# Performance work log

Hardware: AMD Instinct MI355X
Metric: run time of the kernel (lower is better)

Reference implementation:

```python
import jax, jax.numpy as jnp
import numpy as np

D_MODEL = 1024
N_HEADS = 16
POINT_DIM = 4
PLUCKER_DIM = 6
PAIRS4 = [(0, 1), (0, 2), (0, 3), (1, 2), (1, 3), (2, 3)]
_J6 = jnp.array([[0, 0, 0, 0, 0, 1], [0, 0, 0, 0, -1, 0], [0, 0, 0, 1, 0, 0],
                 [0, 0, 1, 0, 0, 0], [0, -1, 0, 0, 0, 0], [1, 0, 0, 0, 0, 0]], dtype=jnp.float32)


def exterior(p1, p2):
    # p1, p2: [..., point_dim] -> normalized Plucker coords [..., 6]
    L = jnp.stack([p1[..., i] * p2[..., j] - p1[..., j] * p2[..., i] for i, j in PAIRS4], axis=-1)
    n = jnp.linalg.norm(L, axis=-1, keepdims=True)
    return L / jnp.maximum(n, 1e-12)


def setup_inputs() -> dict:
    key = jax.random.key(0)
    ks = jax.random.split(key, 16)
    B, T, D, H, pd = 2, 1024, D_MODEL, N_HEADS, POINT_DIM
    s = 0.02
    return {
        "x": jax.random.normal(ks[0], (B, T, D), dtype=jnp.float32),
        "qkv_w": jax.random.normal(ks[1], (D, 3 * D), dtype=jnp.float32) * s,
        "qkv_b": jnp.zeros((3 * D,), dtype=jnp.float32),
        "w1_write_w": jax.random.normal(ks[2], (2 * D, pd * H), dtype=jnp.float32) * s,
        "w2_write_w": jax.random.normal(ks[3], (D, pd * H), dtype=jnp.float32) * s,
        "w1_read_w": jax.random.normal(ks[4], (D, pd * H), dtype=jnp.float32) * s,
        "w2_read_w": jax.random.normal(ks[5], (D, pd * H), dtype=jnp.float32) * s,
        "mem_value_w": jax.random.normal(ks[6], (D, D), dtype=jnp.float32) * s,
        "mem_value_b": jnp.zeros((D,), dtype=jnp.float32),
        "mem_gate_w": jax.random.normal(ks[7], (D, H), dtype=jnp.float32) * s,
        "mem_gate_b": jnp.zeros((H,), dtype=jnp.float32),
        "mem_scale": jnp.full((H,), 0.1, dtype=jnp.float32),
        "out_w": jax.random.normal(ks[8], (D, D), dtype=jnp.float32) * s,
        "out_b": jnp.zeros((D,), dtype=jnp.float32),
        "decay_logits": jnp.full((H,), 4.6, dtype=jnp.float32),
        "J": _J6,
    }


def reference(x, qkv_w, qkv_b, w1_write_w, w2_write_w, w1_read_w, w2_read_w,
              mem_value_w, mem_value_b, mem_gate_w, mem_gate_b, mem_scale,
              out_w, out_b, decay_logits, J):
    B, T, D = x.shape
    H = N_HEADS
    dh = D // H
    pd = POINT_DIM
    scale = dh ** (-0.5)

    # ---- standard causal attention ----
    qkv = (x @ qkv_w + qkv_b).reshape(B, T, 3, H, dh)
    q = jnp.transpose(qkv[:, :, 0], (0, 2, 1, 3))  # [B,H,T,dh]
    k = jnp.transpose(qkv[:, :, 1], (0, 2, 1, 3))
    v = jnp.transpose(qkv[:, :, 2], (0, 2, 1, 3))
    scores = jnp.einsum('bhtd,bhsd->bhts', q, k) * scale
    causal_mask = jnp.triu(jnp.ones((T, T), dtype=bool), k=1)
    scores = jnp.where(causal_mask, -jnp.inf, scores)
    attn = jax.nn.softmax(scores, axis=-1)
    seq_out = jnp.einsum('bhts,bhsd->bthd', attn, v).reshape(B, T, D)

    # ---- trigram write lines ----
    z = jnp.zeros((B, 1, D), dtype=x.dtype)
    x_prev1 = jnp.concatenate([z, x[:, :-1]], axis=1)
    x_prev2 = jnp.concatenate([z, z, x[:, :-2]], axis=1)
    trigram_ctx = jnp.concatenate([x_prev2, x_prev1], axis=-1)  # [B,T,2D]
    w1 = (trigram_ctx @ w1_write_w).reshape(B, T, H, pd)
    w2 = (x @ w2_write_w).reshape(B, T, H, pd)
    write_lines = exterior(w1, w2)  # [B,T,H,6]
    r1 = (x @ w1_read_w).reshape(B, T, H, pd)
    r2 = (x @ w2_read_w).reshape(B, T, H, pd)
    read_lines = exterior(r1, r2)  # [B,T,H,6]

    # ---- Plucker incidence + decay weighting ----
    J_write = jnp.einsum('bshi,ij->bshj', write_lines, J)
    incidence = jnp.einsum('bthi,bshi->bhts', read_lines, J_write)  # [B,H,T,T]
    incidence_sq = incidence ** 2
    positions = jnp.arange(T, dtype=x.dtype)
    diffs = positions[:, None] - positions[None, :]  # [T,T]
    decays = jax.nn.sigmoid(decay_logits)  # [H]
    # strictly-causal (diffs>0) decay weights; masked_fill(triu diag=0, 0) == (diffs>0)
    weights = jnp.where(diffs[None] > 0, decays[:, None, None] ** jnp.maximum(diffs, 0.0)[None], 0.0)
    mem_score = jnp.sum(incidence_sq * weights[None], axis=-1)  # [B,H,T]

    # ---- gated memory value ----
    mem_val = x @ mem_value_w + mem_value_b  # [B,T,D]
    gate = jax.nn.sigmoid(x @ mem_gate_w + mem_gate_b)  # [B,T,H]
    mem_score_t = jnp.transpose(mem_score, (0, 2, 1))  # [B,T,H]
    gated = jax.nn.sigmoid(mem_score_t * mem_scale[None, None, :]) * gate
    gated = jnp.mean(gated, axis=-1, keepdims=True)  # [B,T,1]

    return (seq_out + gated * mem_val) @ out_w + out_b
```

## Files before the change

### kernel.cpp

```cpp
#include <hip/hip_runtime.h>
#include <hip/hip_bf16.h>
#include <stdint.h>


typedef __attribute__((ext_vector_type(8))) __bf16 bf16v8;
typedef __attribute__((ext_vector_type(8))) short  s16x8;
typedef __attribute__((ext_vector_type(4))) float  f32x4;

#define LOG2E 1.4426950408889634f

__device__ __forceinline__ float bf2f(short s) {
  union { uint32_t u; float f; } cv; cv.u = ((uint32_t)(uint16_t)s) << 16; return cv.f;
}
__device__ __forceinline__ short f2bf(float f) {
  union { float f; uint32_t u; } cv; cv.f = f;
  uint32_t r = cv.u + 0x7fffu + ((cv.u >> 16) & 1u);
  return (short)(r >> 16);
}

__device__ __forceinline__ f32x4 mfma_bf16(s16x8 a, s16x8 b, f32x4 c) {
  return __builtin_amdgcn_mfma_f32_16x16x32_bf16(
      __builtin_bit_cast(bf16v8, a), __builtin_bit_cast(bf16v8, b), c, 0, 0, 0);
}

__device__ __forceinline__ void gload_lds16(const void* g, void* l) {
  __builtin_amdgcn_global_load_lds(
      (const __attribute__((address_space(1))) uint32_t*)g,
      (__attribute__((address_space(3))) uint32_t*)l, 16, 0, 0);
}


__global__ void k_cvt(const float* __restrict__ in, short* __restrict__ out, int n) {
  int i = (blockIdx.x * 256 + threadIdx.x) * 4;
  if (i < n) {
    float4 v = *(const float4*)&in[i];
    short4 o;
    o.x = f2bf(v.x); o.y = f2bf(v.y); o.z = f2bf(v.z); o.w = f2bf(v.w);
    *(short4*)&out[i] = o;
  }
}

__global__ void k_tconv(const float* __restrict__ W, short* __restrict__ Wt, int K, int N) {
  __shared__ float tile[32][33];
  const int n0 = blockIdx.x * 32, k0 = blockIdx.y * 32;
  const int tx = threadIdx.x, ty = threadIdx.y;
#pragma unroll
  for (int i = 0; i < 4; i++)
    tile[ty + i * 8][tx] = W[(size_t)(k0 + ty + i * 8) * N + n0 + tx];
  __syncthreads();
#pragma unroll
  for (int i = 0; i < 4; i++)
    Wt[(size_t)(n0 + ty + i * 8) * K + k0 + tx] = f2bf(tile[tx][ty + i * 8]);
}

__global__ void k_smallw(const float* __restrict__ w1w, const float* __restrict__ w2w,
                         const float* __restrict__ r1w, const float* __restrict__ r2w,
                         const float* __restrict__ gw, const float* __restrict__ qkvb,
                         const float* __restrict__ mvb, short* __restrict__ out,
                         float* __restrict__ biasAll) {
  if (blockIdx.x >= 1536) {
    const int i = (blockIdx.x - 1536) * 256 + threadIdx.x;
    if (i < 4480) {
      float v = 0.f;
      if (i < 3072) v = qkvb[i];
      else if (i < 4096) v = mvb[i - 3072];
      biasAll[i] = v;
    }
    return;
  }
  const int idx = blockIdx.x * 256 + threadIdx.x;
  const int r = idx >> 10, k = idx & 1023;
  float v = 0.f;
  if (r < 64)       v = w1w[(size_t)k * 64 + r];
  else if (r < 128) v = w1w[(size_t)(1024 + k) * 64 + (r - 64)];
  else if (r < 192) v = w2w[(size_t)k * 64 + (r - 128)];
  else if (r < 256) v = r1w[(size_t)k * 64 + (r - 192)];
  else if (r < 320) v = r2w[(size_t)k * 64 + (r - 256)];
  else if (r < 336) v = gw[(size_t)k * 16 + (r - 320)];
  out[idx] = f2bf(v);
}


__global__ __launch_bounds__(256) void k_gemmF(const short* __restrict__ A,
                                               const short* __restrict__ Bt,
                                               short* __restrict__ C,
                                               const float* __restrict__ bias,
                                               float* __restrict__ projf) {
  const int N = 4480, K = 1024;
  __shared__ short As[128 * 32];
  __shared__ short Bs[128 * 32];
  const int m0 = blockIdx.x * 128, n0 = blockIdx.y * 128;
  const int tid = threadIdx.x;
  const int lane = tid & 63, w = tid >> 6;
  const int wr = (w >> 1) * 64, wc = (w & 1) * 64;
  const int l15 = lane & 15, lg = lane >> 4;
  f32x4 acc[4][4] = {};
  for (int k0 = 0; k0 < K; k0 += 32) {
#pragma unroll
    for (int p = 0; p < 2; p++) {
      const int e = p * 256 + tid;
      const int r = e >> 2, c8 = (e & 3) << 3;
      gload_lds16(A + (size_t)(m0 + r) * K + k0 + c8, As + e * 8);
      gload_lds16(Bt + (size_t)(n0 + r) * K + k0 + c8, Bs + e * 8);
    }
    __syncthreads();
    s16x8 af[4], bfv[4];
#pragma unroll
    for (int i = 0; i < 4; i++) {
      af[i]  = *(const s16x8*)&As[(wr + i * 16 + l15) * 32 + lg * 8];
      bfv[i] = *(const s16x8*)&Bs[(wc + i * 16 + l15) * 32 + lg * 8];
    }
#pragma unroll
    for (int mi = 0; mi < 4; mi++)
#pragma unroll
      for (int ni = 0; ni < 4; ni++)
        acc[mi][ni] = mfma_bf16(af[mi], bfv[ni], acc[mi][ni]);
    __syncthreads();
  }
  const bool isproj = (n0 >= 4096);
#pragma unroll
  for (int mi = 0; mi < 4; mi++)
#pragma unroll
    for (int ni = 0; ni < 4; ni++) {
      const int col = n0 + wc + ni * 16 + l15;
      const float bv = bias[col];
#pragma unroll
      for (int r = 0; r < 4; r++) {
        const int row = m0 + wr + mi * 16 + lg * 4 + r;
        const float v = acc[mi][ni][r] + bv;
        if (isproj) projf[(size_t)row * 384 + (col - 4096)] = v;
        else        C[(size_t)row * 4480 + col] = f2bf(v);
      }
    }
}


__global__ __launch_bounds__(256) void k_gemm(const short* __restrict__ A,
                                              const short* __restrict__ Bt,
                                              float* __restrict__ C,
                                              const float* __restrict__ bias,
                                              int N, int K) {
  __shared__ short As[128 * 32];
  __shared__ short Bs[128 * 32];
  const int m0 = blockIdx.x * 128, n0 = blockIdx.y * 128;
  const int tid = threadIdx.x;
  const int lane = tid & 63, w = tid >> 6;
  const int wr = (w >> 1) * 64, wc = (w & 1) * 64;
  const int l15 = lane & 15, lg = lane >> 4;
  f32x4 acc[4][4] = {};
  for (int k0 = 0; k0 < K; k0 += 32) {
#pragma unroll
    for (int p = 0; p < 2; p++) {
      const int e = p * 256 + tid;
      const int r = e >> 2, c8 = (e & 3) << 3;
      gload_lds16(A + (size_t)(m0 + r) * K + k0 + c8, As + e * 8);
      gload_lds16(Bt + (size_t)(n0 + r) * K + k0 + c8, Bs + e * 8);
    }
    __syncthreads();
    s16x8 af[4], bfv[4];
#pragma unroll
    for (int i = 0; i < 4; i++) {
      af[i]  = *(const s16x8*)&As[(wr + i * 16 + l15) * 32 + lg * 8];
      bfv[i] = *(const s16x8*)&Bs[(wc + i * 16 + l15) * 32 + lg * 8];
    }
#pragma unroll
    for (int mi = 0; mi < 4; mi++)
#pragma unroll
      for (int ni = 0; ni < 4; ni++)
        acc[mi][ni] = mfma_bf16(af[mi], bfv[ni], acc[mi][ni]);
    __syncthreads();
  }
#pragma unroll
  for (int mi = 0; mi < 4; mi++)
#pragma unroll
    for (int ni = 0; ni < 4; ni++) {
      const int col = n0 + wc + ni * 16 + l15;
      const float bv = bias ? bias[col] : 0.f;
#pragma unroll
      for (int r = 0; r < 4; r++) {
        const int row = m0 + wr + mi * 16 + lg * 4 + r;
        C[(size_t)row * N + col] = acc[mi][ni][r] + bv;
      }
    }
}


__global__ void k_vtr(const short* __restrict__ fused, short* __restrict__ vtg) {
  __shared__ short tile[32][33];
  const int bh = blockIdx.z;
  const int b = bh >> 4, h = bh & 15;
  const int t0 = blockIdx.x * 32, d0 = blockIdx.y * 32;
  const int tx = threadIdx.x, ty = threadIdx.y;
#pragma unroll
  for (int i = 0; i < 4; i++)
    tile[ty + i * 8][tx] =
        fused[(size_t)(b * 1024 + t0 + ty + i * 8) * 4480 + 2048 + h * 64 + d0 + tx];
  __syncthreads();
#pragma unroll
  for (int i = 0; i < 4; i++)
    vtg[(size_t)(bh * 64 + d0 + ty + i * 8) * 1024 + t0 + tx] = tile[tx][ty + i * 8];
}


__global__ __launch_bounds__(256) void k_attn(const short* __restrict__ fused,
                                              const short* __restrict__ vtg,
                                              short* __restrict__ outp) {
  const int id = blockIdx.x;
  const int phase = id >> 8;
  const int v = id & 255;
  const int bh = (v & 7) + 8 * ((v >> 3) & 3);
  const int jx = v >> 5;
  const int j = phase ? jx : (15 - jx);
  const int b = bh >> 4, h = bh & 15;
  const int tid = threadIdx.x, lane = tid & 63, w = tid >> 6;
  const int l15 = lane & 15, lg = lane >> 4;
  const int q0 = j * 64;
  const int nkv = j + 1;

  __shared__ short Kl[2][64 * 72];
  __shared__ short Vt[2][64 * 72];
  __shared__ short Pl[4][16 * 72];
  const short* base = fused + (size_t)b * 1024 * 4480;
  const short* vbase = vtg + (size_t)bh * 64 * 1024;
  short* op = outp + (size_t)b * 1024 * 1024;

  const int e0 = tid, e1 = tid + 256;
  const int r0e = e0 >> 3, c0e = (e0 & 7) << 3;
  const int r1e = e1 >> 3, c1e = (e1 & 7) << 3;

  s16x8 qf[2];
#pragma unroll
  for (int ks = 0; ks < 2; ks++)
    qf[ks] = *(const s16x8*)&base[(size_t)(q0 + w * 16 + l15) * 4480 +
                                  h * 64 + ks * 32 + lg * 8];

  f32x4 O[4] = {};
  float m_run[4], l_run[4];
#pragma unroll
  for (int r = 0; r < 4; r++) { m_run[r] = -1e30f; l_run[r] = 0.f; }

  {
    s16x8 ka = *(const s16x8*)&base[(size_t)r0e * 4480 + 1024 + h * 64 + c0e];
    s16x8 kb = *(const s16x8*)&base[(size_t)r1e * 4480 + 1024 + h * 64 + c1e];
    s16x8 va = *(const s16x8*)&vbase[(size_t)r0e * 1024 + c0e];
    s16x8 vb = *(const s16x8*)&vbase[(size_t)r1e * 1024 + c1e];
    *(s16x8*)&Kl[0][r0e * 72 + c0e] = ka;
    *(s16x8*)&Kl[0][r1e * 72 + c1e] = kb;
    *(s16x8*)&Vt[0][r0e * 72 + c0e] = va;
    *(s16x8*)&Vt[0][r1e * 72 + c1e] = vb;
  }
  __syncthreads();

  for (int kt = 0; kt < nkv; kt++) {
    const int cur = kt & 1;
    const int kv0 = kt * 64;
    const bool pf = (kt + 1 < nkv);
    s16x8 kn0, kn1, vn0, vn1;
    if (pf) {
      const int kvn = kv0 + 64;
      kn0 = *(const s16x8*)&base[(size_t)(kvn + r0e) * 4480 + 1024 + h * 64 + c0e];
      kn1 = *(const s16x8*)&base[(size_t)(kvn + r1e) * 4480 + 1024 + h * 64 + c1e];
      vn0 = *(const s16x8*)&vbase[(size_t)r0e * 1024 + kvn + c0e];
      vn1 = *(const s16x8*)&vbase[(size_t)r1e * 1024 + kvn + c1e];
    }

    f32x4 S[4] = {};
    __builtin_amdgcn_s_setprio(1);
#pragma unroll
    for (int sf = 0; sf < 4; sf++) {
      s16x8 kf0 = *(const s16x8*)&Kl[cur][(sf * 16 + l15) * 72 + lg * 8];
      s16x8 kf1 = *(const s16x8*)&Kl[cur][(sf * 16 + l15) * 72 + 32 + lg * 8];
      S[sf] = mfma_bf16(qf[0], kf0, S[sf]);
      S[sf] = mfma_bf16(qf[1], kf1, S[sf]);
    }
    __builtin_amdgcn_s_setprio(0);

    const bool diag = (kt == j);
    float sv[4][4];
#pragma unroll
    for (int sf = 0; sf < 4; sf++)
#pragma unroll
      for (int r = 0; r < 4; r++) {
        float vv = S[sf][r] * 0.125f;
        if (diag) {
          const int sg = kv0 + sf * 16 + l15;
          const int qg = q0 + w * 16 + lg * 4 + r;
          if (sg > qg) vv = -1e30f;
        }
        sv[sf][r] = vv;
      }
#pragma unroll
    for (int r = 0; r < 4; r++) {
      float pm = fmaxf(fmaxf(sv[0][r], sv[1][r]), fmaxf(sv[2][r], sv[3][r]));
      pm = fmaxf(pm, __shfl_xor(pm, 1, 64));
      pm = fmaxf(pm, __shfl_xor(pm, 2, 64));
      pm = fmaxf(pm, __shfl_xor(pm, 4, 64));
      pm = fmaxf(pm, __shfl_xor(pm, 8, 64));
      const float mn = fmaxf(m_run[r], pm);
      const float fac = exp2f((m_run[r] - mn) * LOG2E);
      m_run[r] = mn;
      float rs = 0.f;
#pragma unroll
      for (int sf = 0; sf < 4; sf++) {
        float p = (sv[sf][r] <= -1e29f) ? 0.f : exp2f((sv[sf][r] - mn) * LOG2E);
        rs += p;
        Pl[w][(lg * 4 + r) * 72 + sf * 16 + l15] = f2bf(p);
      }
      rs += __shfl_xor(rs, 1, 64);
      rs += __shfl_xor(rs, 2, 64);
      rs += __shfl_xor(rs, 4, 64);
      rs += __shfl_xor(rs, 8, 64);
      l_run[r] = l_run[r] * fac + rs;
#pragma unroll
      for (int nf = 0; nf < 4; nf++) O[nf][r] *= fac;
    }

    __builtin_amdgcn_s_setprio(1);
#pragma unroll
    for (int ks = 0; ks < 2; ks++) {
      s16x8 pfr = *(const s16x8*)&Pl[w][l15 * 72 + ks * 32 + lg * 8];
#pragma unroll
      for (int nf = 0; nf < 4; nf++) {
        s16x8 vf = *(const s16x8*)&Vt[cur][(nf * 16 + l15) * 72 + ks * 32 + lg * 8];
        O[nf] = mfma_bf16(pfr, vf, O[nf]);
      }
    }
    __builtin_amdgcn_s_setprio(0);

    __syncthreads();
    if (pf) {
      const int nxt = cur ^ 1;
      *(s16x8*)&Kl[nxt][r0e * 72 + c0e] = kn0;
      *(s16x8*)&Kl[nxt][r1e * 72 + c1e] = kn1;
      *(s16x8*)&Vt[nxt][r0e * 72 + c0e] = vn0;
      *(s16x8*)&Vt[nxt][r1e * 72 + c1e] = vn1;
      __syncthreads();
    }
  }

#pragma unroll
  for (int nf = 0; nf < 4; nf++)
#pragma unroll
    for (int r = 0; r < 4; r++) {
      const int row = q0 + w * 16 + lg * 4 + r;
      op[(size_t)row * 1024 + h * 64 + nf * 16 + l15] = f2bf(O[nf][r] / l_run[r]);
    }
}


__device__ __forceinline__ void exterior6(const float p1[4], const float p2[4], float L[6]) {
  L[0] = p1[0] * p2[1] - p1[1] * p2[0];
  L[1] = p1[0] * p2[2] - p1[2] * p2[0];
  L[2] = p1[0] * p2[3] - p1[3] * p2[0];
  L[3] = p1[1] * p2[2] - p1[2] * p2[1];
  L[4] = p1[1] * p2[3] - p1[3] * p2[1];
  L[5] = p1[2] * p2[3] - p1[3] * p2[2];
  float n = sqrtf(L[0] * L[0] + L[1] * L[1] + L[2] * L[2] +
                  L[3] * L[3] + L[4] * L[4] + L[5] * L[5]);
  float inv = 1.f / fmaxf(n, 1e-12f);
#pragma unroll
  for (int j = 0; j < 6; j++) L[j] *= inv;
}

__global__ void k_lines(const float* __restrict__ proj, const float* __restrict__ Jm,
                        float* __restrict__ jw, float* __restrict__ rl) {
  const int idx = blockIdx.x * 256 + threadIdx.x;
  const int t = idx & 1023, h = (idx >> 10) & 15, b = idx >> 14;
  const int n = b * 1024 + t;
  const int bh = b * 16 + h;
  float p1[4], p2[4], L[6];
#pragma unroll
  for (int p = 0; p < 4; p++) {
    float a  = (t >= 2) ? proj[(size_t)(n - 2) * 384 + h * 4 + p] : 0.f;
    float bb = (t >= 1) ? proj[(size_t)(n - 1) * 384 + 64 + h * 4 + p] : 0.f;
    p1[p] = a + bb;
    p2[p] = proj[(size_t)n * 384 + 128 + h * 4 + p];
  }
  exterior6(p1, p2, L);
  const size_t jo = (size_t)bh * 6144 + t;
#pragma unroll
  for (int j = 0; j < 6; j++) {
    float s = 0.f;
#pragma unroll
    for (int i = 0; i < 6; i++) s += L[i] * Jm[i * 6 + j];
    jw[jo + (size_t)j * 1024] = s;
  }
#pragma unroll
  for (int p = 0; p < 4; p++) {
    p1[p] = proj[(size_t)n * 384 + 192 + h * 4 + p];
    p2[p] = proj[(size_t)n * 384 + 256 + h * 4 + p];
  }
  exterior6(p1, p2, L);
  const size_t ro = ((size_t)bh * 1024 + t) * 6;
#pragma unroll
  for (int j = 0; j < 6; j++) rl[ro + j] = L[j];
}


__global__ __launch_bounds__(256) void k_mscore(const float* __restrict__ jw,
                                                const float* __restrict__ rl,
                                                const float* __restrict__ dlog,
                                                float* __restrict__ ms) {
  const int gtid = blockIdx.x * 256 + threadIdx.x;
  const int wid = gtid >> 6, lane = gtid & 63;
  const int bh = wid >> 10, t = wid & 1023;
  const int h = bh & 15, b = bh >> 4;
  const float d = 1.f / (1.f + expf(-dlog[h]));
  const float l2d = log2f(d);
  const float* jwp = jw + (size_t)bh * 6144;
  const float* rp = rl + ((size_t)bh * 1024 + t) * 6;
  const float r0 = rp[0], r1 = rp[1], r2 = rp[2], r3 = rp[3], r4 = rp[4], r5 = rp[5];
  float wgt = exp2f((float)(t - lane) * l2d);
  const float gw = exp2f(-64.f * l2d);
  float acc = 0.f;
  for (int s = lane; s < t; s += 64) {
    const float dot = r0 * jwp[s] + r1 * jwp[1024 + s] + r2 * jwp[2048 + s] +
                      r3 * jwp[3072 + s] + r4 * jwp[4096 + s] + r5 * jwp[5120 + s];
    acc += wgt * dot * dot;
    wgt *= gw;
  }
  acc += __shfl_xor(acc, 1, 64);
  acc += __shfl_xor(acc, 2, 64);
  acc += __shfl_xor(acc, 4, 64);
  acc += __shfl_xor(acc, 8, 64);
  acc += __shfl_xor(acc, 16, 64);
  acc += __shfl_xor(acc, 32, 64);
  if (lane == 0) ms[((size_t)(b * 1024 + t)) * 16 + h] = acc;
}


__global__ __launch_bounds__(256) void k_combine(const short* __restrict__ attn,
                                                 const short* __restrict__ fused,
                                                 const float* __restrict__ proj,
                                                 const float* __restrict__ ms,
                                                 const float* __restrict__ mem_scale,
                                                 const float* __restrict__ gate_b,
                                                 short* __restrict__ comb) {
  const int n = blockIdx.x;
  const int tid = threadIdx.x;
  __shared__ float gsh;
  if (tid < 16) {
    const float gp = proj[(size_t)n * 384 + 320 + tid] + gate_b[tid];
    const float g = 1.f / (1.f + expf(-gp));
    const float sc = ms[(size_t)n * 16 + tid] * mem_scale[tid];
    const float sg = 1.f / (1.f + expf(-sc));
    float v = sg * g;
    v += __shfl_xor(v, 1, 64);
    v += __shfl_xor(v, 2, 64);
    v += __shfl_xor(v, 4, 64);
    v += __shfl_xor(v, 8, 64);
    if (tid == 0) gsh = v * (1.f / 16.f);
  }
  __syncthreads();
  const float g = gsh;
  const int c0 = tid * 4;
  short4 av = *(const short4*)&attn[(size_t)n * 1024 + c0];
  short4 mvv = *(const short4*)&fused[(size_t)n * 4480 + 3072 + c0];
  short4 ov;
  ov.x = f2bf(bf2f(av.x) + g * bf2f(mvv.x));
  ov.y = f2bf(bf2f(av.y) + g * bf2f(mvv.y));
  ov.z = f2bf(bf2f(av.z) + g * bf2f(mvv.z));
  ov.w = f2bf(bf2f(av.w) + g * bf2f(mvv.w));
  *(short4*)&comb[(size_t)n * 1024 + c0] = ov;
}


extern "C" void kernel_launch(void* const* d_in, const int* in_sizes, int n_in,
                              void* d_out, int out_size, void* d_ws, size_t ws_size,
                              hipStream_t stream) {
  const float* x    = (const float*)d_in[0];
  const float* qkvw = (const float*)d_in[1];
  const float* qkvb = (const float*)d_in[2];
  const float* w1w  = (const float*)d_in[3];
  const float* w2w  = (const float*)d_in[4];
  const float* r1w  = (const float*)d_in[5];
  const float* r2w  = (const float*)d_in[6];
  const float* mvw  = (const float*)d_in[7];
  const float* mvb  = (const float*)d_in[8];
  const float* gw   = (const float*)d_in[9];
  const float* gb   = (const float*)d_in[10];
  const float* msc  = (const float*)d_in[11];
  const float* ow   = (const float*)d_in[12];
  const float* ob   = (const float*)d_in[13];
  const float* dlog = (const float*)d_in[14];
  const float* Jm   = (const float*)d_in[15];
  float* out = (float*)d_out;

  char* wsp = (char*)d_ws;
  auto alloc = [&](size_t bytes) {
    char* p = wsp;
    wsp += (bytes + 255) & ~(size_t)255;
    return p;
  };
  short* xb     = (short*)alloc((size_t)2048 * 1024 * 2);
  short* btall  = (short*)alloc((size_t)4480 * 1024 * 2);
  short* owT    = (short*)alloc((size_t)1024 * 1024 * 2);
  short* fusedC = (short*)alloc((size_t)2048 * 4480 * 2);
  float* projf  = (float*)alloc((size_t)2048 * 384 * 4);
  float* biasA  = (float*)alloc((size_t)4480 * 4);
  short* vtg    = (short*)alloc((size_t)32 * 64 * 1024 * 2);
  short* attnO  = (short*)alloc((size_t)2048 * 1024 * 2);
  short* comb   = (short*)alloc((size_t)2048 * 1024 * 2);
  float* jwb    = (float*)alloc((size_t)32 * 6144 * 4);
  float* rlb    = (float*)alloc((size_t)32768 * 6 * 4);
  float* msb    = (float*)alloc((size_t)2048 * 16 * 4);

  k_cvt<<<2048, 256, 0, stream>>>(x, xb, 2048 * 1024);
  dim3 tb(32, 8);
  k_tconv<<<dim3(96, 32), tb, 0, stream>>>(qkvw, btall, 1024, 3072);
  k_tconv<<<dim3(32, 32), tb, 0, stream>>>(mvw, btall + (size_t)3072 * 1024, 1024, 1024);
  k_tconv<<<dim3(32, 32), tb, 0, stream>>>(ow, owT, 1024, 1024);
  k_smallw<<<1554, 256, 0, stream>>>(w1w, w2w, r1w, r2w, gw, qkvb, mvb,
                                     btall + (size_t)4096 * 1024, biasA);

  k_gemmF<<<dim3(16, 35), 256, 0, stream>>>(xb, btall, fusedC, biasA, projf);

  k_vtr<<<dim3(32, 2, 32), tb, 0, stream>>>(fusedC, vtg);
  k_attn<<<512, 256, 0, stream>>>(fusedC, vtg, attnO);

  k_lines<<<128, 256, 0, stream>>>(projf, Jm, jwb, rlb);
  k_mscore<<<8192, 256, 0, stream>>>(jwb, rlb, dlog, msb);
  k_combine<<<2048, 256, 0, stream>>>(attnO, fusedC, projf, msb, msc, gb, comb);

  k_gemm<<<dim3(16, 8), 256, 0, stream>>>(comb, owT, out, ob, 1024, 1024);
}
```

Before: 143.7 us.

## Split attention KV range across two blocks, merge partials, fuse prep kernels

Attention now runs as 1024 blocks, each handling half of a query tile's causal KV range. A new merge kernel combines the two float partial outputs using their saved max and sum statistics, which shortens the longest blocks and raises parallelism. The online softmax now rescales only when the running max grows by more than a threshold, and the LDS K/V tiles are single-buffered. The five weight and input conversion launches are folded into one prep kernel to cut launch overhead, at the cost of extra float partial traffic and a further launch for the merge.

```diff
diff --git a/kernel.cpp b/kernel.cpp
--- a/kernel.cpp
+++ b/kernel.cpp
@@ -30,54 +30,65 @@
 }
 
 
-__global__ void k_cvt(const float* __restrict__ in, short* __restrict__ out, int n) {
-  int i = (blockIdx.x * 256 + threadIdx.x) * 4;
-  if (i < n) {
-    float4 v = *(const float4*)&in[i];
+__global__ __launch_bounds__(256) void k_prep(
+    const float* __restrict__ x, const float* __restrict__ qkvw,
+    const float* __restrict__ mvw, const float* __restrict__ ow,
+    const float* __restrict__ w1w, const float* __restrict__ w2w,
+    const float* __restrict__ r1w, const float* __restrict__ r2w,
+    const float* __restrict__ gw, const float* __restrict__ qkvb,
+    const float* __restrict__ mvb,
+    short* __restrict__ xb, short* __restrict__ btall, short* __restrict__ owT,
+    float* __restrict__ biasAll) {
+  __shared__ float tile[32][33];
+  const int bid = blockIdx.x;
+  const int tid = threadIdx.x;
+  if (bid < 2048) {
+    const int i = (bid * 256 + tid) * 4;
+    float4 v = *(const float4*)&x[i];
     short4 o;
     o.x = f2bf(v.x); o.y = f2bf(v.y); o.z = f2bf(v.z); o.w = f2bf(v.w);
-    *(short4*)&out[i] = o;
-  }
-}
-
-__global__ void k_tconv(const float* __restrict__ W, short* __restrict__ Wt, int K, int N) {
-  __shared__ float tile[32][33];
-  const int n0 = blockIdx.x * 32, k0 = blockIdx.y * 32;
-  const int tx = threadIdx.x, ty = threadIdx.y;
-#pragma unroll
-  for (int i = 0; i < 4; i++)
-    tile[ty + i * 8][tx] = W[(size_t)(k0 + ty + i * 8) * N + n0 + tx];
-  __syncthreads();
-#pragma unroll
-  for (int i = 0; i < 4; i++)
-    Wt[(size_t)(n0 + ty + i * 8) * K + k0 + tx] = f2bf(tile[tx][ty + i * 8]);
-}
-
-__global__ void k_smallw(const float* __restrict__ w1w, const float* __restrict__ w2w,
-                         const float* __restrict__ r1w, const float* __restrict__ r2w,
-                         const float* __restrict__ gw, const float* __restrict__ qkvb,
-                         const float* __restrict__ mvb, short* __restrict__ out,
-                         float* __restrict__ biasAll) {
-  if (blockIdx.x >= 1536) {
-    const int i = (blockIdx.x - 1536) * 256 + threadIdx.x;
+    *(short4*)&xb[i] = o;
+    return;
+  }
+  if (bid < 7168) {
+    const float* W; short* Wt; int N, u;
+    if (bid < 5120)      { W = qkvw; Wt = btall;                       N = 3072; u = bid - 2048; }
+    else if (bid < 6144) { W = mvw;  Wt = btall + (size_t)3072 * 1024; N = 1024; u = bid - 5120; }
+    else                 { W = ow;   Wt = owT;                         N = 1024; u = bid - 6144; }
+    const int ntiles = N >> 5;
+    const int n0 = (u % ntiles) * 32, k0 = (u / ntiles) * 32;
+    const int tx = tid & 31, ty = tid >> 5;
+#pragma unroll
+    for (int i = 0; i < 4; i++)
+      tile[ty + i * 8][tx] = W[(size_t)(k0 + ty + i * 8) * N + n0 + tx];
+    __syncthreads();
+#pragma unroll
+    for (int i = 0; i < 4; i++)
+      Wt[(size_t)(n0 + ty + i * 8) * 1024 + k0 + tx] = f2bf(tile[tx][ty + i * 8]);
+    return;
+  }
+  if (bid < 8704) {
+    const int idx = (bid - 7168) * 256 + tid;
+    const int r = idx >> 10, k = idx & 1023;
+    float v = 0.f;
+    if (r < 64)       v = w1w[(size_t)k * 64 + r];
+    else if (r < 128) v = w1w[(size_t)(1024 + k) * 64 + (r - 64)];
+    else if (r < 192) v = w2w[(size_t)k * 64 + (r - 128)];
+    else if (r < 256) v = r1w[(size_t)k * 64 + (r - 192)];
+    else if (r < 320) v = r2w[(size_t)k * 64 + (r - 256)];
+    else if (r < 336) v = gw[(size_t)k * 16 + (r - 320)];
+    btall[(size_t)4096 * 1024 + idx] = f2bf(v);
+    return;
+  }
+  {
+    const int i = (bid - 8704) * 256 + tid;
     if (i < 4480) {
       float v = 0.f;
       if (i < 3072) v = qkvb[i];
       else if (i < 4096) v = mvb[i - 3072];
       biasAll[i] = v;
     }
-    return;
-  }
-  const int idx = blockIdx.x * 256 + threadIdx.x;
-  const int r = idx >> 10, k = idx & 1023;
-  float v = 0.f;
-  if (r < 64)       v = w1w[(size_t)k * 64 + r];
-  else if (r < 128) v = w1w[(size_t)(1024 + k) * 64 + (r - 64)];
-  else if (r < 192) v = w2w[(size_t)k * 64 + (r - 128)];
-  else if (r < 256) v = r1w[(size_t)k * 64 + (r - 192)];
-  else if (r < 320) v = r2w[(size_t)k * 64 + (r - 256)];
-  else if (r < 336) v = gw[(size_t)k * 16 + (r - 320)];
-  out[idx] = f2bf(v);
+  }
 }
 
 
@@ -204,25 +215,27 @@
 
 __global__ __launch_bounds__(256) void k_attn(const short* __restrict__ fused,
                                               const short* __restrict__ vtg,
-                                              short* __restrict__ outp) {
+                                              float* __restrict__ Of,
+                                              float* __restrict__ Ml) {
   const int id = blockIdx.x;
-  const int phase = id >> 8;
-  const int v = id & 255;
-  const int bh = (v & 7) + 8 * ((v >> 3) & 3);
-  const int jx = v >> 5;
-  const int j = phase ? jx : (15 - jx);
+  const int j = 15 - (id >> 6);
+  const int rem = id & 63;
+  const int sid = rem >> 5, bh = rem & 31;
   const int b = bh >> 4, h = bh & 15;
   const int tid = threadIdx.x, lane = tid & 63, w = tid >> 6;
   const int l15 = lane & 15, lg = lane >> 4;
   const int q0 = j * 64;
   const int nkv = j + 1;
-
-  __shared__ short Kl[2][64 * 72];
-  __shared__ short Vt[2][64 * 72];
+  const int half = (nkv + 1) >> 1;
+  const int lo = sid ? half : 0;
+  const int hi = sid ? nkv : half;
+  const int pidx = ((j * 32 + bh) << 1) | sid;
+
+  __shared__ short Kl[64 * 72];
+  __shared__ short Vt[64 * 72];
   __shared__ short Pl[4][16 * 72];
   const short* base = fused + (size_t)b * 1024 * 4480;
   const short* vbase = vtg + (size_t)bh * 64 * 1024;
-  short* op = outp + (size_t)b * 1024 * 1024;
 
   const int e0 = tid, e1 = tid + 256;
   const int r0e = e0 >> 3, c0e = (e0 & 7) << 3;
@@ -239,22 +252,22 @@
 #pragma unroll
   for (int r = 0; r < 4; r++) { m_run[r] = -1e30f; l_run[r] = 0.f; }
 
-  {
-    s16x8 ka = *(const s16x8*)&base[(size_t)r0e * 4480 + 1024 + h * 64 + c0e];
-    s16x8 kb = *(const s16x8*)&base[(size_t)r1e * 4480 + 1024 + h * 64 + c1e];
-    s16x8 va = *(const s16x8*)&vbase[(size_t)r0e * 1024 + c0e];
-    s16x8 vb = *(const s16x8*)&vbase[(size_t)r1e * 1024 + c1e];
-    *(s16x8*)&Kl[0][r0e * 72 + c0e] = ka;
-    *(s16x8*)&Kl[0][r1e * 72 + c1e] = kb;
-    *(s16x8*)&Vt[0][r0e * 72 + c0e] = va;
-    *(s16x8*)&Vt[0][r1e * 72 + c1e] = vb;
+  if (lo < hi) {
+    const int kv0 = lo * 64;
+    s16x8 ka = *(const s16x8*)&base[(size_t)(kv0 + r0e) * 4480 + 1024 + h * 64 + c0e];
+    s16x8 kb = *(const s16x8*)&base[(size_t)(kv0 + r1e) * 4480 + 1024 + h * 64 + c1e];
+    s16x8 va = *(const s16x8*)&vbase[(size_t)r0e * 1024 + kv0 + c0e];
+    s16x8 vb = *(const s16x8*)&vbase[(size_t)r1e * 1024 + kv0 + c1e];
+    *(s16x8*)&Kl[r0e * 72 + c0e] = ka;
+    *(s16x8*)&Kl[r1e * 72 + c1e] = kb;
+    *(s16x8*)&Vt[r0e * 72 + c0e] = va;
+    *(s16x8*)&Vt[r1e * 72 + c1e] = vb;
   }
   __syncthreads();
 
-  for (int kt = 0; kt < nkv; kt++) {
-    const int cur = kt & 1;
+  for (int kt = lo; kt < hi; kt++) {
     const int kv0 = kt * 64;
-    const bool pf = (kt + 1 < nkv);
+    const bool pf = (kt + 1 < hi);
     s16x8 kn0, kn1, vn0, vn1;
     if (pf) {
       const int kvn = kv0 + 64;
@@ -268,8 +281,8 @@
     __builtin_amdgcn_s_setprio(1);
 #pragma unroll
     for (int sf = 0; sf < 4; sf++) {
-      s16x8 kf0 = *(const s16x8*)&Kl[cur][(sf * 16 + l15) * 72 + lg * 8];
-      s16x8 kf1 = *(const s16x8*)&Kl[cur][(sf * 16 + l15) * 72 + 32 + lg * 8];
+      s16x8 kf0 = *(const s16x8*)&Kl[(sf * 16 + l15) * 72 + lg * 8];
+      s16x8 kf1 = *(const s16x8*)&Kl[(sf * 16 + l15) * 72 + 32 + lg * 8];
       S[sf] = mfma_bf16(qf[0], kf0, S[sf]);
       S[sf] = mfma_bf16(qf[1], kf1, S[sf]);
     }
@@ -296,13 +309,17 @@
       pm = fmaxf(pm, __shfl_xor(pm, 2, 64));
       pm = fmaxf(pm, __shfl_xor(pm, 4, 64));
       pm = fmaxf(pm, __shfl_xor(pm, 8, 64));
-      const float mn = fmaxf(m_run[r], pm);
-      const float fac = exp2f((m_run[r] - mn) * LOG2E);
-      m_run[r] = mn;
+      if (pm > m_run[r] + 8.f) {
+        const float fac = exp2f((m_run[r] - pm) * LOG2E);
+        m_run[r] = pm;
+        l_run[r] *= fac;
+#pragma unroll
+        for (int nf = 0; nf < 4; nf++) O[nf][r] *= fac;
+      }
       float rs = 0.f;
 #pragma unroll
       for (int sf = 0; sf < 4; sf++) {
-        float p = (sv[sf][r] <= -1e29f) ? 0.f : exp2f((sv[sf][r] - mn) * LOG2E);
+        float p = (sv[sf][r] <= -1e29f) ? 0.f : exp2f((sv[sf][r] - m_run[r]) * LOG2E);
         rs += p;
         Pl[w][(lg * 4 + r) * 72 + sf * 16 + l15] = f2bf(p);
       }
@@ -310,9 +327,7 @@
       rs += __shfl_xor(rs, 2, 64);
       rs += __shfl_xor(rs, 4, 64);
       rs += __shfl_xor(rs, 8, 64);
-      l_run[r] = l_run[r] * fac + rs;
-#pragma unroll
-      for (int nf = 0; nf < 4; nf++) O[nf][r] *= fac;
+      l_run[r] += rs;
     }
 
     __builtin_amdgcn_s_setprio(1);
@@ -321,7 +336,7 @@
       s16x8 pfr = *(const s16x8*)&Pl[w][l15 * 72 + ks * 32 + lg * 8];
 #pragma unroll
       for (int nf = 0; nf < 4; nf++) {
-        s16x8 vf = *(const s16x8*)&Vt[cur][(nf * 16 + l15) * 72 + ks * 32 + lg * 8];
+        s16x8 vf = *(const s16x8*)&Vt[(nf * 16 + l15) * 72 + ks * 32 + lg * 8];
         O[nf] = mfma_bf16(pfr, vf, O[nf]);
       }
     }
@@ -329,22 +344,55 @@
 
     __syncthreads();
     if (pf) {
-      const int nxt = cur ^ 1;
-      *(s16x8*)&Kl[nxt][r0e * 72 + c0e] = kn0;
-      *(s16x8*)&Kl[nxt][r1e * 72 + c1e] = kn1;
-      *(s16x8*)&Vt[nxt][r0e * 72 + c0e] = vn0;
-      *(s16x8*)&Vt[nxt][r1e * 72 + c1e] = vn1;
+      *(s16x8*)&Kl[r0e * 72 + c0e] = kn0;
+      *(s16x8*)&Kl[r1e * 72 + c1e] = kn1;
+      *(s16x8*)&Vt[r0e * 72 + c0e] = vn0;
+      *(s16x8*)&Vt[r1e * 72 + c1e] = vn1;
       __syncthreads();
     }
   }
 
-#pragma unroll
-  for (int nf = 0; nf < 4; nf++)
-#pragma unroll
-    for (int r = 0; r < 4; r++) {
-      const int row = q0 + w * 16 + lg * 4 + r;
-      op[(size_t)row * 1024 + h * 64 + nf * 16 + l15] = f2bf(O[nf][r] / l_run[r]);
-    }
+  float* ob = Of + (size_t)pidx * 4096;
+  float* mb = Ml + (size_t)pidx * 128;
+#pragma unroll
+  for (int r = 0; r < 4; r++) {
+    const int rloc = w * 16 + lg * 4 + r;
+#pragma unroll
+    for (int nf = 0; nf < 4; nf++)
+      ob[rloc * 64 + nf * 16 + l15] = O[nf][r];
+    if (l15 == 0) {
+      mb[rloc] = m_run[r];
+      mb[64 + rloc] = l_run[r];
+    }
+  }
+}
+
+
+__global__ __launch_bounds__(256) void k_amerge(const float* __restrict__ Of,
+                                                const float* __restrict__ Ml,
+                                                short* __restrict__ outp) {
+  const int g = blockIdx.x * 256 + threadIdx.x;
+  const int rg = g >> 4, c4 = (g & 15) << 2;
+  const int p = rg >> 6, rloc = rg & 63;
+  const int j = p >> 5, bh = p & 31;
+  const int b = bh >> 4, h = bh & 15;
+  const int t = j * 64 + rloc;
+  const float* ml0 = Ml + (size_t)(p * 2 + 0) * 128;
+  const float* ml1 = Ml + (size_t)(p * 2 + 1) * 128;
+  const float m0 = ml0[rloc], l0 = ml0[64 + rloc];
+  const float m1 = ml1[rloc], l1 = ml1[64 + rloc];
+  const float M = fmaxf(m0, m1);
+  const float w0 = exp2f((m0 - M) * LOG2E);
+  const float w1 = exp2f((m1 - M) * LOG2E);
+  const float inv = 1.f / (w0 * l0 + w1 * l1);
+  f32x4 o0 = *(const f32x4*)&Of[(size_t)(p * 2 + 0) * 4096 + rloc * 64 + c4];
+  f32x4 o1 = *(const f32x4*)&Of[(size_t)(p * 2 + 1) * 4096 + rloc * 64 + c4];
+  short4 ov;
+  ov.x = f2bf((w0 * o0[0] + w1 * o1[0]) * inv);
+  ov.y = f2bf((w0 * o0[1] + w1 * o1[1]) * inv);
+  ov.z = f2bf((w0 * o0[2] + w1 * o1[2]) * inv);
+  ov.w = f2bf((w0 * o0[3] + w1 * o1[3]) * inv);
+  *(short4*)&outp[((size_t)(b * 1024 + t)) * 1024 + h * 64 + c4] = ov;
 }
 
 
@@ -504,19 +552,17 @@
   float* jwb    = (float*)alloc((size_t)32 * 6144 * 4);
   float* rlb    = (float*)alloc((size_t)32768 * 6 * 4);
   float* msb    = (float*)alloc((size_t)2048 * 16 * 4);
-
-  k_cvt<<<2048, 256, 0, stream>>>(x, xb, 2048 * 1024);
-  dim3 tb(32, 8);
-  k_tconv<<<dim3(96, 32), tb, 0, stream>>>(qkvw, btall, 1024, 3072);
-  k_tconv<<<dim3(32, 32), tb, 0, stream>>>(mvw, btall + (size_t)3072 * 1024, 1024, 1024);
-  k_tconv<<<dim3(32, 32), tb, 0, stream>>>(ow, owT, 1024, 1024);
-  k_smallw<<<1554, 256, 0, stream>>>(w1w, w2w, r1w, r2w, gw, qkvb, mvb,
-                                     btall + (size_t)4096 * 1024, biasA);
+  float* Of     = (float*)alloc((size_t)1024 * 4096 * 4);
+  float* Mlb    = (float*)alloc((size_t)1024 * 128 * 4);
+
+  k_prep<<<8722, 256, 0, stream>>>(x, qkvw, mvw, ow, w1w, w2w, r1w, r2w, gw,
+                                   qkvb, mvb, xb, btall, owT, biasA);
 
   k_gemmF<<<dim3(16, 35), 256, 0, stream>>>(xb, btall, fusedC, biasA, projf);
 
-  k_vtr<<<dim3(32, 2, 32), tb, 0, stream>>>(fusedC, vtg);
-  k_attn<<<512, 256, 0, stream>>>(fusedC, vtg, attnO);
+  k_vtr<<<dim3(32, 2, 32), dim3(32, 8), 0, stream>>>(fusedC, vtg);
+  k_attn<<<1024, 256, 0, stream>>>(fusedC, vtg, Of, Mlb);
+  k_amerge<<<2048, 256, 0, stream>>>(Of, Mlb, attnO);
 
   k_lines<<<128, 256, 0, stream>>>(projf, Jm, jwb, rlb);
   k_mscore<<<8192, 256, 0, stream>>>(jwb, rlb, dlog, msb);
```

Result: faster. 135.9 us (-5.5%).
